# Performance work log

Measured on AMD Instinct MI355X. Metric: run time of the kernel, lower is better.

## Reference

```python
import jax, jax.numpy as jnp
import numpy as np

D, DFF, H, K = 512, 2048, 8, 31
DK = D // H
EPS = 1e-5


def _ln(x, g, b):
    m = jnp.mean(x, axis=-1, keepdims=True)
    v = jnp.mean((x - m) ** 2, axis=-1, keepdims=True)
    return (x - m) * jax.lax.rsqrt(v + EPS) * g + b


def _ffn(x, w1, b1, w2, b2):
    return jax.nn.silu(x @ w1 + b1) @ w2 + b2


def _rel_shift(x):
    # x: (B, H, T, P) with P = 2T-1
    b, h, q, p = x.shape
    x = jnp.pad(x, ((0, 0), (0, 0), (0, 0), (1, 0)))
    x = x.reshape(b, h, p + 1, q)[:, :, 1:, :]
    return x.reshape(b, h, q, p)


def setup_inputs() -> dict:
    key = jax.random.key(0)
    ks = jax.random.split(key, 32)
    r = lambda i, shape: 0.02 * jax.random.normal(ks[i], shape, dtype=jnp.float32)
    B, T = 4, 1024
    inp = {
        'x': jax.random.normal(ks[0], (B, T, D), dtype=jnp.float32),
        'pos_emb': jax.random.normal(ks[1], (1, 2 * T - 1, D), dtype=jnp.float32),
        # LayerNorms (5)
        'ln1_g': jnp.ones((D,)), 'ln1_b': jnp.zeros((D,)),
        'ln2_g': jnp.ones((D,)), 'ln2_b': jnp.zeros((D,)),
        'ln3_g': jnp.ones((D,)), 'ln3_b': jnp.zeros((D,)),
        'ln4_g': jnp.ones((D,)), 'ln4_b': jnp.zeros((D,)),
        'ln5_g': jnp.ones((D,)), 'ln5_b': jnp.zeros((D,)),
        # FFN1
        'ff1_w1': r(2, (D, DFF)), 'ff1_b1': jnp.zeros((DFF,)),
        'ff1_w2': r(3, (DFF, D)), 'ff1_b2': jnp.zeros((D,)),
        # Attention
        'wq': r(4, (D, D)), 'bq': jnp.zeros((D,)),
        'wk': r(5, (D, D)), 'bk': jnp.zeros((D,)),
        'wv': r(6, (D, D)), 'bv': jnp.zeros((D,)),
        'wp': r(7, (D, D)),
        'wo': r(8, (D, D)), 'bo': jnp.zeros((D,)),
        'pos_u': r(9, (H, DK)), 'pos_v': r(10, (H, DK)),
        # Conv module
        'pw1_w': r(11, (2 * D, D)), 'pw1_b': jnp.zeros((2 * D,)),
        'dw_w': r(12, (D, 1, K)), 'dw_b': jnp.zeros((D,)),
        'bn_g': jnp.ones((D,)), 'bn_b': jnp.zeros((D,)),
        'pw2_w': r(13, (D, D)), 'pw2_b': jnp.zeros((D,)),
        # FFN2
        'ff2_w1': r(14, (D, DFF)), 'ff2_b1': jnp.zeros((DFF,)),
        'ff2_w2': r(15, (DFF, D)), 'ff2_b2': jnp.zeros((D,)),
    }
    return inp


def _attn(x, pos_emb, wq, bq, wk, bk, wv, bv, wp, wo, bo, pos_u, pos_v):
    B, T, _ = x.shape
    q = (x @ wq + bq).reshape(B, T, H, DK).transpose(0, 2, 1, 3)
    k = (x @ wk + bk).reshape(B, T, H, DK).transpose(0, 2, 1, 3)
    v = (x @ wv + bv).reshape(B, T, H, DK).transpose(0, 2, 1, 3)
    P = pos_emb.shape[1]
    p = (pos_emb[0] @ wp).reshape(P, H, DK)  # (P, H, DK)
    ac = jnp.einsum('bhqd,bhkd->bhqk', q + pos_u[:, None, :], k)
    bd = jnp.einsum('bhqd,phd->bhqp', q + pos_v[:, None, :], p)
    bd = _rel_shift(bd)[:, :, :, :T]
    scores = (ac + bd) * (DK ** -0.5)
    attn = jax.nn.softmax(scores, axis=-1)
    out = jnp.einsum('bhqk,bhkd->bhqd', attn, v)
    out = out.transpose(0, 2, 1, 3).reshape(B, T, D)
    return out @ wo + bo


def _conv(x, pw1_w, pw1_b, dw_w, dw_b, bn_g, bn_b, pw2_w, pw2_b):
    y = x.transpose(0, 2, 1)  # (B, D, T)
    y = jnp.einsum('od,bdt->bot', pw1_w, y) + pw1_b[:, None]
    a, g = jnp.split(y, 2, axis=1)
    y = a * jax.nn.sigmoid(g)  # GLU
    pad = (K - 1) // 2
    y = jax.lax.conv_general_dilated(
        y, dw_w, (1,), [(pad, pad)],
        dimension_numbers=('NCW', 'OIW', 'NCW'), feature_group_count=D)
    y = y + dw_b[:, None]
    m = jnp.mean(y, axis=(0, 2), keepdims=True)
    var = jnp.mean((y - m) ** 2, axis=(0, 2), keepdims=True)
    y = (y - m) * jax.lax.rsqrt(var + EPS) * bn_g[:, None] + bn_b[:, None]
    y = jax.nn.silu(y)
    y = jnp.einsum('od,bdt->bot', pw2_w, y) + pw2_b[:, None]
    return y.transpose(0, 2, 1)


def reference(x, pos_emb,
              ln1_g, ln1_b, ff1_w1, ff1_b1, ff1_w2, ff1_b2,
              ln2_g, ln2_b, wq, bq, wk, bk, wv, bv, wp, wo, bo, pos_u, pos_v,
              ln3_g, ln3_b, pw1_w, pw1_b, dw_w, dw_b, bn_g, bn_b, pw2_w, pw2_b,
              ln4_g, ln4_b, ff2_w1, ff2_b1, ff2_w2, ff2_b2,
              ln5_g, ln5_b):
    h = x + 0.5 * _ffn(_ln(x, ln1_g, ln1_b), ff1_w1, ff1_b1, ff1_w2, ff1_b2)
    h = h + _attn(_ln(h, ln2_g, ln2_b), pos_emb, wq, bq, wk, bk, wv, bv, wp, wo, bo, pos_u, pos_v)
    h = h + _conv(_ln(h, ln3_g, ln3_b), pw1_w, pw1_b, dw_w, dw_b, bn_g, bn_b, pw2_w, pw2_b)
    h = h + 0.5 * _ffn(_ln(h, ln4_g, ln4_b), ff2_w1, ff2_b1, ff2_w2, ff2_b2)
    return _ln(h, ln5_g, ln5_b)
```

## Files before the change

### kernel.cpp

```cpp
#include <hip/hip_runtime.h>
#include <math.h>

#define TT   1024
#define BBZ  4
#define DD   512
#define DFF_ 2048
#define HH   8
#define DKK  64
#define NTOK 4096
#define EPSF 1e-5f
#define MB   1048576
#define QSCALE 0.18033688011112042f
#define M0OFF  24.0f

typedef unsigned short u16;
typedef __attribute__((ext_vector_type(8))) short s8v;
typedef __attribute__((ext_vector_type(4))) float f32x4;
typedef __attribute__((ext_vector_type(4))) unsigned short us4;

__device__ __forceinline__ float b2f(u16 v){
    union { unsigned int u; float f; } x; x.u = ((unsigned int)v) << 16; return x.f;
}
__device__ __forceinline__ u16 f2b(float f){
    union { float f; unsigned int u; } x; x.f = f;
    unsigned int r = x.u + 0x7fffu + ((x.u >> 16) & 1u);
    return (u16)(r >> 16);
}
__device__ __forceinline__ float sigmoidf_(float x){ return 1.0f/(1.0f+__expf(-x)); }

__device__ __forceinline__ void gld16(const u16* g, u16* l){
    __builtin_amdgcn_global_load_lds(
        (const __attribute__((address_space(1))) unsigned int*)g,
        (__attribute__((address_space(3))) unsigned int*)l, 16, 0, 0);
}

template<int OMODE>
__global__ __launch_bounds__(256) void bgemm128(
    const u16* __restrict__ A, int lda,
    const u16* __restrict__ B, int ldb,
    void* __restrict__ Cv, int ldc, int K,
    const float* __restrict__ bias, int act, float alpha,
    const float* __restrict__ resid,
    const float* __restrict__ posu, const float* __restrict__ posv)
{
    int n0 = blockIdx.x * 128;
    int m0 = blockIdx.y * 128;

    __shared__ u16 As[128*64];
    __shared__ u16 Bs[128*64];

    int t = threadIdx.x;
    int w = t >> 6, l = t & 63;
    int lrow = l >> 3, lslot = l & 7;
    int kswz = (lslot ^ lrow) * 8;
    int wm = w >> 1, wn = w & 1;
    int lr = l & 15, lk = l >> 4;

    f32x4 acc[4][4] = {};

    for (int k0 = 0; k0 < K; k0 += 64){
        #pragma unroll
        for (int it = 0; it < 4; ++it){
            int rb = it*32 + w*8;
            gld16(A + (size_t)(m0 + rb + lrow)*lda + k0 + kswz, &As[rb*64]);
            gld16(B + (size_t)(n0 + rb + lrow)*ldb + k0 + kswz, &Bs[rb*64]);
        }
        __syncthreads();

        s8v af[2][4], bf[2][4];
        #pragma unroll
        for (int kh = 0; kh < 2; ++kh){
            int sl = (kh*4 + lk) ^ (lr & 7);
            #pragma unroll
            for (int mi = 0; mi < 4; ++mi)
                af[kh][mi] = *(const s8v*)&As[(wm*64 + mi*16 + lr)*64 + sl*8];
            #pragma unroll
            for (int ni = 0; ni < 4; ++ni)
                bf[kh][ni] = *(const s8v*)&Bs[(wn*64 + ni*16 + lr)*64 + sl*8];
        }
        #pragma unroll
        for (int kh = 0; kh < 2; ++kh)
            #pragma unroll
            for (int mi = 0; mi < 4; ++mi)
                #pragma unroll
                for (int ni = 0; ni < 4; ++ni)
                    acc[mi][ni] = __builtin_amdgcn_mfma_f32_16x16x32_bf16(
                        af[kh][mi], bf[kh][ni], acc[mi][ni], 0, 0, 0);
        __syncthreads();
    }

    #pragma unroll
    for (int mi = 0; mi < 4; ++mi){
        #pragma unroll
        for (int ni = 0; ni < 4; ++ni){
            int gn = n0 + wn*64 + ni*16 + lr;
            float bval = bias ? bias[gn] : 0.0f;
            #pragma unroll
            for (int r = 0; r < 4; ++r){
                int gm = m0 + wm*64 + mi*16 + lk*4 + r;
                float vv = acc[mi][ni][r] + bval;
                if (act) vv = vv * sigmoidf_(vv);
                if (OMODE == 0){
                    vv *= alpha;
                    if (resid) vv += resid[(size_t)gm*ldc + gn];
                    ((float*)Cv)[(size_t)gm*ldc + gn] = vv;
                } else if (OMODE == 1){
                    ((u16*)Cv)[(size_t)gm*ldc + gn] = f2b(vv);
                } else if (OMODE == 5){
                    u16* base = (u16*)Cv;
                    if (gn < 512){
                        size_t idx = (size_t)gm*512 + gn;
                        base[idx]              = f2b((vv + posu[gn])*QSCALE);
                        base[idx + (2u<<20)]   = f2b((vv + posv[gn])*QSCALE);
                    } else if (gn < 1024){
                        base[(4u<<20) + (size_t)gm*512 + (gn-512)] = f2b(vv);
                    } else {
                        int gnp = gn - 1024;
                        int bb = gm >> 10, tt2 = gm & 1023;
                        size_t idx = (((size_t)(bb*8 + (gnp>>6)))*64 + (gnp&63))*1024 + tt2;
                        base[(6u<<20) + idx] = f2b(vv);
                    }
                } else {
                    u16* base = (u16*)Cv;
                    size_t idx = (gn < 512)
                        ? ((size_t)gm*512 + gn)*2
                        : ((size_t)gm*512 + (gn-512))*2 + 1;
                    base[idx] = f2b(vv);
                }
            }
        }
    }
}

template<int OMODE>
__global__ __launch_bounds__(256) void bgemm64(
    const u16* __restrict__ A, int lda,
    const u16* __restrict__ B, int ldb,
    void* __restrict__ Cv, int ldc, int K,
    const float* __restrict__ bias, float alpha,
    const float* __restrict__ resid)
{
    int n0 = blockIdx.x * 64;
    int m0 = blockIdx.y * 64;

    __shared__ u16 As[64*64];
    __shared__ u16 Bs[64*64];

    int t = threadIdx.x;
    int w = t >> 6, l = t & 63;
    int lrow = l >> 3, lslot = l & 7;
    int kswz = (lslot ^ lrow) * 8;
    int wm = w >> 1, wn = w & 1;
    int lr = l & 15, lk = l >> 4;

    f32x4 acc[2][2] = {};

    for (int k0 = 0; k0 < K; k0 += 64){
        #pragma unroll
        for (int it = 0; it < 2; ++it){
            int rb = it*32 + w*8;
            gld16(A + (size_t)(m0 + rb + lrow)*lda + k0 + kswz, &As[rb*64]);
            gld16(B + (size_t)(n0 + rb + lrow)*ldb + k0 + kswz, &Bs[rb*64]);
        }
        __syncthreads();

        s8v af[2][2], bf[2][2];
        #pragma unroll
        for (int kh = 0; kh < 2; ++kh){
            int sl = (kh*4 + lk) ^ (lr & 7);
            #pragma unroll
            for (int mi = 0; mi < 2; ++mi)
                af[kh][mi] = *(const s8v*)&As[(wm*32 + mi*16 + lr)*64 + sl*8];
            #pragma unroll
            for (int ni = 0; ni < 2; ++ni)
                bf[kh][ni] = *(const s8v*)&Bs[(wn*32 + ni*16 + lr)*64 + sl*8];
        }
        #pragma unroll
        for (int kh = 0; kh < 2; ++kh)
            #pragma unroll
            for (int mi = 0; mi < 2; ++mi)
                #pragma unroll
                for (int ni = 0; ni < 2; ++ni)
                    acc[mi][ni] = __builtin_amdgcn_mfma_f32_16x16x32_bf16(
                        af[kh][mi], bf[kh][ni], acc[mi][ni], 0, 0, 0);
        __syncthreads();
    }

    #pragma unroll
    for (int mi = 0; mi < 2; ++mi){
        #pragma unroll
        for (int ni = 0; ni < 2; ++ni){
            int gn = n0 + wn*32 + ni*16 + lr;
            float bval = bias ? bias[gn] : 0.0f;
            #pragma unroll
            for (int r = 0; r < 4; ++r){
                int gm = m0 + wm*32 + mi*16 + lk*4 + r;
                float vv = acc[mi][ni][r] + bval;
                if (OMODE == 0){
                    vv *= alpha;
                    if (resid) vv += resid[(size_t)gm*ldc + gn];
                    ((float*)Cv)[(size_t)gm*ldc + gn] = vv;
                } else {
                    ((u16*)Cv)[(size_t)gm*ldc + gn] = f2b(vv);
                }
            }
        }
    }
}

__global__ __launch_bounds__(256) void bgemm64k(
    const u16* __restrict__ A, int lda,
    const u16* __restrict__ B, int ldb,
    float* __restrict__ C, int ldc, int K,
    const float* __restrict__ bias, float alpha,
    const float* __restrict__ resid)
{
    int n0 = blockIdx.x * 64;
    int m0 = blockIdx.y * 64;

    __shared__ u16 As[64*128];
    __shared__ u16 Bs[64*128];

    int t = threadIdx.x;
    int w = t >> 6, l = t & 63;
    int r4 = l >> 4;
    int s16 = l & 15;
    int kswz = (s16 ^ (w*4 + r4)) * 8;
    int wm = w >> 1, wn = w & 1;
    int lr = l & 15, lk = l >> 4;

    f32x4 acc[2][2] = {};

    for (int k0 = 0; k0 < K; k0 += 128){
        #pragma unroll
        for (int cb = 0; cb < 4; ++cb){
            int rowu = cb*16 + w*4;
            gld16(A + (size_t)(m0 + rowu + r4)*lda + k0 + kswz, &As[rowu*128]);
            gld16(B + (size_t)(n0 + rowu + r4)*ldb + k0 + kswz, &Bs[rowu*128]);
        }
        __syncthreads();

        #pragma unroll
        for (int kh = 0; kh < 4; ++kh){
            int sl = ((kh*4 + lk) ^ lr) * 8;
            s8v af[2], bf[2];
            #pragma unroll
            for (int mi = 0; mi < 2; ++mi)
                af[mi] = *(const s8v*)&As[(wm*32 + mi*16 + lr)*128 + sl];
            #pragma unroll
            for (int ni = 0; ni < 2; ++ni)
                bf[ni] = *(const s8v*)&Bs[(wn*32 + ni*16 + lr)*128 + sl];
            #pragma unroll
            for (int mi = 0; mi < 2; ++mi)
                #pragma unroll
                for (int ni = 0; ni < 2; ++ni)
                    acc[mi][ni] = __builtin_amdgcn_mfma_f32_16x16x32_bf16(
                        af[mi], bf[ni], acc[mi][ni], 0, 0, 0);
        }
        __syncthreads();
    }

    #pragma unroll
    for (int mi = 0; mi < 2; ++mi){
        #pragma unroll
        for (int ni = 0; ni < 2; ++ni){
            int gn = n0 + wn*32 + ni*16 + lr;
            float bval = bias ? bias[gn] : 0.0f;
            #pragma unroll
            for (int r = 0; r < 4; ++r){
                int gm = m0 + wm*32 + mi*16 + lk*4 + r;
                float vv = (acc[mi][ni][r] + bval) * alpha;
                if (resid) vv += resid[(size_t)gm*ldc + gn];
                C[(size_t)gm*ldc + gn] = vv;
            }
        }
    }
}

__global__ __launch_bounds__(256) void attn_fused(
    const u16* __restrict__ qub, const u16* __restrict__ qvb,
    const u16* __restrict__ kb,  const u16* __restrict__ vt,
    const u16* __restrict__ pp,  u16* __restrict__ out)
{
    int z = blockIdx.y;
    int b = z >> 3, hh = z & 7;
    int i0 = blockIdx.x * 64;

    __shared__ u16 Kb2[2][64*64];
    __shared__ u16 Vb2[2][64*64];
    __shared__ u16 Pring[3][64*64];
    __shared__ u16 PT[64*64];
    __shared__ float Band[64*64];

    int t = threadIdx.x;
    int w = t >> 6, l = t & 63;
    int lrow = l >> 3, lslot = l & 7;
    int kswz = (lslot ^ lrow) * 8;
    int lr = l & 15, lk = l >> 4;

    #pragma unroll
    for (int it = 0; it < 2; ++it){
        int rb = it*32 + w*8;
        gld16(qub + (size_t)(b*TT + i0 + rb + lrow)*DD + hh*64 + kswz, &PT[rb*64]);
        gld16(qvb + (size_t)(b*TT + i0 + rb + lrow)*DD + hh*64 + kswz,
              (u16*)Band + rb*64);
    }
    __syncthreads();
    s8v af_u[2], af_v[2];
    #pragma unroll
    for (int kh = 0; kh < 2; ++kh){
        int sl = (kh*4 + lk) ^ (lr & 7);
        af_u[kh] = *(const s8v*)&PT[(w*16 + lr)*64 + sl*8];
        af_v[kh] = *(const s8v*)((const u16*)Band + (w*16 + lr)*64 + sl*8);
    }
    #pragma unroll
    for (int it = 0; it < 2; ++it){
        int rb = it*32 + w*8;
        gld16(kb + (size_t)(b*TT +        rb + lrow)*DD + hh*64 + kswz, &Kb2[0][rb*64]);
        gld16(vt + ((size_t)z*64 + rb + lrow)*TT +                kswz, &Vb2[0][rb*64]);
        gld16(pp + (size_t)(960  - i0 +   rb + lrow)*DD + hh*64 + kswz, &Pring[0][rb*64]);
        gld16(pp + (size_t)(1024 - i0 +   rb + lrow)*DD + hh*64 + kswz, &Pring[1][rb*64]);
    }

    f32x4 o_[4] = {};
    float Lp[4] = {0.f, 0.f, 0.f, 0.f};

    int nbase = 3 - w;
    int s0 = 0, s1 = 1, s2 = 2;

    for (int jt = 0; jt < 16; ++jt){
        int cur = jt & 1;
        __syncthreads();

        if (jt < 15){
            #pragma unroll
            for (int it = 0; it < 2; ++it){
                int rb = it*32 + w*8;
                gld16(kb + (size_t)(b*TT + (jt+1)*64 + rb + lrow)*DD + hh*64 + kswz,
                      &Kb2[cur^1][rb*64]);
                gld16(vt + ((size_t)z*64 + rb + lrow)*TT + (jt+1)*64 + kswz,
                      &Vb2[cur^1][rb*64]);
                gld16(pp + (size_t)(960 + (jt+2)*64 - i0 + rb + lrow)*DD + hh*64 + kswz,
                      &Pring[s2][rb*64]);
            }
        }

        f32x4 sac[4] = {};
        f32x4 g[5] = {};
        __builtin_amdgcn_s_setprio(1);
        #pragma unroll
        for (int kh = 0; kh < 2; ++kh){
            int sl = (kh*4 + lk) ^ (lr & 7);
            #pragma unroll
            for (int n = 0; n < 4; ++n){
                s8v bK = *(const s8v*)&Kb2[cur][(n*16 + lr)*64 + sl*8];
                sac[n] = __builtin_amdgcn_mfma_f32_16x16x32_bf16(af_u[kh], bK, sac[n], 0,0,0);
            }
            #pragma unroll
            for (int n = 0; n < 5; ++n){
                int nn = nbase + n;
                const u16* pc = (nn & 4) ? &Pring[s1][0] : &Pring[s0][0];
                s8v bP = *(const s8v*)&pc[(((nn&3)*16) + lr)*64 + sl*8];
                g[n] = __builtin_amdgcn_mfma_f32_16x16x32_bf16(af_v[kh], bP, g[n], 0,0,0);
            }
        }
        __builtin_amdgcn_s_setprio(0);
        #pragma unroll
        for (int n = 0; n < 5; ++n){
            int nn = nbase + n;
            #pragma unroll
            for (int r = 0; r < 4; ++r){
                int ii = w*16 + lk*4 + r;
                int jj = nn*16 + lr - 63 + ii;
                if (jj >= 0 && jj < 64)
                    Band[ii*64 + ((jj + 4*ii) & 63)] = g[n][r];
            }
        }

        float p_[4][4];
        #pragma unroll
        for (int r = 0; r < 4; ++r){
            int ii = w*16 + lk*4 + r;
            float rs = 0.0f;
            #pragma unroll
            for (int n = 0; n < 4; ++n){
                int jj = n*16 + lr;
                float s2 = sac[n][r] + Band[ii*64 + ((jj + 4*ii) & 63)];
                float pv = __builtin_amdgcn_exp2f(s2 - M0OFF);
                p_[n][r] = pv; rs += pv;
            }
            Lp[r] += rs;
        }

        #pragma unroll
        for (int n = 0; n < 4; ++n)
            #pragma unroll
            for (int r = 0; r < 4; ++r){
                int ii  = w*16 + lk*4 + r;
                int col = n*16 + lr;
                int sl  = (col>>3) ^ (ii&7);
                PT[ii*64 + sl*8 + (col&7)] = f2b(p_[n][r]);
            }

        __builtin_amdgcn_s_setprio(1);
        #pragma unroll
        for (int kh = 0; kh < 2; ++kh){
            int sl = (kh*4 + lk) ^ (lr & 7);
            s8v ap = *(const s8v*)&PT[(w*16 + lr)*64 + sl*8];
            #pragma unroll
            for (int n = 0; n < 4; ++n){
                s8v bV = *(const s8v*)&Vb2[cur][(n*16 + lr)*64 + sl*8];
                o_[n] = __builtin_amdgcn_mfma_f32_16x16x32_bf16(ap, bV, o_[n], 0,0,0);
            }
        }
        __builtin_amdgcn_s_setprio(0);
        int tmp = s0; s0 = s1; s1 = s2; s2 = tmp;
    }

    float Lr[4];
    #pragma unroll
    for (int r = 0; r < 4; ++r){
        float Lv = Lp[r];
        #pragma unroll
        for (int msk = 1; msk < 16; msk <<= 1) Lv += __shfl_xor(Lv, msk);
        Lr[r] = 1.0f / Lv;
    }

    #pragma unroll
    for (int n = 0; n < 4; ++n)
        #pragma unroll
        for (int r = 0; r < 4; ++r){
            int i  = i0 + w*16 + lk*4 + r;
            int dk = n*16 + lr;
            out[(size_t)(b*TT + i)*DD + hh*64 + dk] = f2b(o_[n][r] * Lr[r]);
        }
}

template<int OB>
__global__ __launch_bounds__(256) void ln_kernel(const float* __restrict__ in,
    const float* __restrict__ g, const float* __restrict__ b, void* __restrict__ outv)
{
    int w = threadIdx.x >> 6, l = threadIdx.x & 63;
    int row = blockIdx.x*4 + w;
    const float4* xr = (const float4*)(in + (size_t)row*DD);
    float4 v0 = xr[l], v1 = xr[64 + l];
    float s = v0.x+v0.y+v0.z+v0.w + v1.x+v1.y+v1.z+v1.w;
    float q = v0.x*v0.x+v0.y*v0.y+v0.z*v0.z+v0.w*v0.w
            + v1.x*v1.x+v1.y*v1.y+v1.z*v1.z+v1.w*v1.w;
    #pragma unroll
    for (int msk = 1; msk < 64; msk <<= 1){
        s += __shfl_xor(s, msk);
        q += __shfl_xor(q, msk);
    }
    float mean = s*(1.0f/DD);
    float var  = q*(1.0f/DD) - mean*mean;
    float inv  = rsqrtf(var+EPSF);
    float4 g0 = ((const float4*)g)[l], g1 = ((const float4*)g)[64+l];
    float4 b0 = ((const float4*)b)[l], b1 = ((const float4*)b)[64+l];
    float y0x=(v0.x-mean)*inv*g0.x+b0.x, y0y=(v0.y-mean)*inv*g0.y+b0.y;
    float y0z=(v0.z-mean)*inv*g0.z+b0.z, y0w=(v0.w-mean)*inv*g0.w+b0.w;
    float y1x=(v1.x-mean)*inv*g1.x+b1.x, y1y=(v1.y-mean)*inv*g1.y+b1.y;
    float y1z=(v1.z-mean)*inv*g1.z+b1.z, y1w=(v1.w-mean)*inv*g1.w+b1.w;
    if (OB){
        us4 o0 = { f2b(y0x), f2b(y0y), f2b(y0z), f2b(y0w) };
        us4 o1 = { f2b(y1x), f2b(y1y), f2b(y1z), f2b(y1w) };
        us4* op = (us4*)((u16*)outv + (size_t)row*DD);
        op[l] = o0; op[64+l] = o1;
    } else {
        float4 o0 = { y0x, y0y, y0z, y0w };
        float4 o1 = { y1x, y1y, y1z, y1w };
        float4* op = (float4*)((float*)outv + (size_t)row*DD);
        op[l] = o0; op[64+l] = o1;
    }
}

struct Prep9 {
    const float* s[9];
    u16* d[9];
    int R[9], C[9];
    int t0[10];
};

__global__ __launch_bounds__(256) void prep_transpose(Prep9 P)
{
    __shared__ float tile[32][33];
    int bid = blockIdx.x;
    int j = 0;
    #pragma unroll
    for (int e=1; e<9; e++) if (bid >= P.t0[e]) j = e;
    int lb = bid - P.t0[j];
    int nx = P.C[j] >> 5;
    int c0 = (lb % nx) << 5;
    int r0 = (lb / nx) << 5;
    const float* in = P.s[j];
    u16* out = P.d[j];
    int R = P.R[j], C = P.C[j];
    int tx = threadIdx.x & 31, ty = threadIdx.x >> 5;
    #pragma unroll
    for (int i=0;i<4;i++){
        int rr = ty + i*8;
        tile[rr][tx] = in[(size_t)(r0+rr)*C + c0+tx];
    }
    __syncthreads();
    #pragma unroll
    for (int i=0;i<4;i++){
        int cc = ty + i*8;
        out[(size_t)(c0+cc)*R + r0+tx] = f2b(tile[tx][cc]);
    }
}

__global__ __launch_bounds__(256) void prep_convert(
    const float* __restrict__ pw1_w, const float* __restrict__ pw2_w,
    const float* __restrict__ pos_emb, const float* __restrict__ dw_w,
    const float* __restrict__ bq, const float* __restrict__ bk,
    const float* __restrict__ bv,
    u16* __restrict__ pw1b, u16* __restrict__ pw2b,
    u16* __restrict__ posb, float* __restrict__ wt, float* __restrict__ bqkv)
{
    int i = blockIdx.x*256 + threadIdx.x;
    if (i < 524288) { pw1b[i] = f2b(pw1_w[i]); return; }
    i -= 524288;
    if (i < 262144) { pw2b[i] = f2b(pw2_w[i]); return; }
    i -= 262144;
    if (i < 1048576) { posb[i] = (i < 2047*512) ? f2b(pos_emb[i]) : (u16)0; return; }
    i -= 1048576;
    if (i < 15872) { int kk = i >> 9, d = i & 511; wt[i] = dw_w[d*31+kk]; return; }
    i -= 15872;
    if (i < 1536) bqkv[i] = (i < 512) ? bq[i] : (i < 1024 ? bk[i-512] : bv[i-1024]);
}

__global__ __launch_bounds__(256) void dwconv_kernel(const unsigned int* __restrict__ t2i,
    const float* __restrict__ wt, const float* __restrict__ bias, u16* __restrict__ z)
{
    int d  = blockIdx.x*256 + threadIdx.x;
    int c  = blockIdx.y;
    int b  = c >> 7;
    int t0 = (c & 127) << 3;
    const unsigned int* pa = t2i + (size_t)b*TT*512 + d;
    float wv[31];
    #pragma unroll
    for (int kk=0;kk<31;kk++) wv[kk] = wt[kk*512 + d];
    float xv[38];
    #pragma unroll
    for (int e=0;e<38;e++){
        int tp = t0 - 15 + e;
        if (tp >= 0 && tp < TT){
            unsigned int pv = pa[(size_t)tp*512];
            float a  = b2f((u16)(pv & 0xffffu));
            float gg = b2f((u16)(pv >> 16));
            xv[e] = a * sigmoidf_(gg);
        } else xv[e] = 0.0f;
    }
    float bsv = bias[d];
    #pragma unroll
    for (int j=0;j<8;j++){
        float sum = bsv;
        #pragma unroll
        for (int kk=0;kk<31;kk++) sum = fmaf(xv[j+kk], wv[kk], sum);
        z[(size_t)(b*TT+t0+j)*DD + d] = f2b(sum);
    }
}

__global__ __launch_bounds__(256) void bn_reduce2(const u16* __restrict__ z,
    float* __restrict__ stats)
{
    int bi = blockIdx.x;
    int t  = threadIdx.x;
    float s0=0.f,q0=0.f,s1=0.f,q1=0.f;
    #pragma unroll
    for (int r=0;r<16;r++){
        size_t row = (size_t)(bi*16 + r)*DD;
        float v0 = b2f(z[row + t]);
        float v1 = b2f(z[row + t + 256]);
        s0 += v0; q0 += v0*v0;
        s1 += v1; q1 += v1*v1;
    }
    atomicAdd(&stats[t],        s0);
    atomicAdd(&stats[512 + t],  q0);
    atomicAdd(&stats[t + 256],      s1);
    atomicAdd(&stats[512 + t + 256], q1);
}

__global__ __launch_bounds__(256) void bn_apply_kernel(const u16* __restrict__ z,
    const float* __restrict__ stats, const float* __restrict__ g, const float* __restrict__ b,
    u16* __restrict__ out)
{
    int idx = blockIdx.x*256 + threadIdx.x;
    int c = idx & (DD-1);
    float m   = stats[c]*(1.0f/NTOK);
    float var = stats[DD+c]*(1.0f/NTOK) - m*m;
    float vv  = (b2f(z[idx])-m)*rsqrtf(var+EPSF)*g[c] + b[c];
    out[idx]  = f2b(vv*sigmoidf_(vv));
}

extern "C" void kernel_launch(void* const* d_in, const int* in_sizes, int n_in,
                              void* d_out, int out_size, void* d_ws, size_t ws_size,
                              hipStream_t stream)
{
    const float* x       = (const float*)d_in[0];
    const float* pos_emb = (const float*)d_in[1];
    const float* ln1_g=(const float*)d_in[2],  *ln1_b=(const float*)d_in[3];
    const float* ln2_g=(const float*)d_in[4],  *ln2_b=(const float*)d_in[5];
    const float* ln3_g=(const float*)d_in[6],  *ln3_b=(const float*)d_in[7];
    const float* ln4_g=(const float*)d_in[8],  *ln4_b=(const float*)d_in[9];
    const float* ln5_g=(const float*)d_in[10], *ln5_b=(const float*)d_in[11];
    const float* ff1_w1=(const float*)d_in[12], *ff1_b1=(const float*)d_in[13];
    const float* ff1_w2=(const float*)d_in[14], *ff1_b2=(const float*)d_in[15];
    const float* wq=(const float*)d_in[16], *bq=(const float*)d_in[17];
    const float* wk=(const float*)d_in[18], *bk=(const float*)d_in[19];
    const float* wv=(const float*)d_in[20], *bv=(const float*)d_in[21];
    const float* wp=(const float*)d_in[22];
    const float* wo=(const float*)d_in[23], *bo=(const float*)d_in[24];
    const float* pos_u=(const float*)d_in[25], *pos_v=(const float*)d_in[26];
    const float* pw1_w=(const float*)d_in[27], *pw1_b=(const float*)d_in[28];
    const float* dw_w=(const float*)d_in[29],  *dw_b=(const float*)d_in[30];
    const float* bn_g=(const float*)d_in[31],  *bn_b=(const float*)d_in[32];
    const float* pw2_w=(const float*)d_in[33], *pw2_b=(const float*)d_in[34];
    const float* ff2_w1=(const float*)d_in[35], *ff2_b1=(const float*)d_in[36];
    const float* ff2_w2=(const float*)d_in[37], *ff2_b2=(const float*)d_in[38];

    char* W = (char*)d_ws;
    float* h    = (float*)(W);
    u16*  xn    = (u16*) (W + (size_t) 8*MB);
    u16*  wall  = (u16*) (W + (size_t)12*MB);
    u16*  qub   = (u16*) (W + (size_t)28*MB);
    u16*  qvb   = (u16*) (W + (size_t)32*MB);
    u16*  kb    = (u16*) (W + (size_t)36*MB);
    u16*  vt    = (u16*) (W + (size_t)40*MB);
    u16*  pproj = (u16*) (W + (size_t)44*MB);
    char* big   = W + (size_t)48*MB;
    u16*  ffh   = (u16*)big;
    unsigned int* t2i = (unsigned int*)big;
    u16*  t3u   = (u16*)(big + (size_t)8*MB);
    float* stats= (float*)(W + (size_t)112*MB);
    float* wt   = stats + 4096;
    float* bqkv = wt + 15872;

    u16* ff1w1T = wall;
    u16* ff1w2T = wall + 1048576;
    u16* wqT    = wall + 2097152;
    u16* wkT    = wall + 2359296;
    u16* wvT    = wall + 2621440;
    u16* wpT    = wall + 2883584;
    u16* woT    = wall + 3145728;
    u16* ff2w1T = wall + 3407872;
    u16* ff2w2T = wall + 4456448;
    u16* pw1b   = wall + 5505024;
    u16* pw2b   = wall + 6029312;
    u16* posb   = wall + 6291456;

    dim3 blk(256);

    Prep9 P;
    P.s[0]=ff1_w1; P.d[0]=ff1w1T; P.R[0]=512;  P.C[0]=2048;
    P.s[1]=ff1_w2; P.d[1]=ff1w2T; P.R[1]=2048; P.C[1]=512;
    P.s[2]=wq;     P.d[2]=wqT;    P.R[2]=512;  P.C[2]=512;
    P.s[3]=wk;     P.d[3]=wkT;    P.R[3]=512;  P.C[3]=512;
    P.s[4]=wv;     P.d[4]=wvT;    P.R[4]=512;  P.C[4]=512;
    P.s[5]=wp;     P.d[5]=wpT;    P.R[5]=512;  P.C[5]=512;
    P.s[6]=wo;     P.d[6]=woT;    P.R[6]=512;  P.C[6]=512;
    P.s[7]=ff2_w1; P.d[7]=ff2w1T; P.R[7]=512;  P.C[7]=2048;
    P.s[8]=ff2_w2; P.d[8]=ff2w2T; P.R[8]=2048; P.C[8]=512;
    int tc[9] = {1024,1024,256,256,256,256,256,1024,1024};
    P.t0[0]=0; for (int e=0;e<9;e++) P.t0[e+1]=P.t0[e]+tc[e];
    prep_transpose<<<dim3(5376), blk, 0, stream>>>(P);
    prep_convert<<<dim3(7236), blk, 0, stream>>>(pw1_w, pw2_w, pos_emb, dw_w,
                                                 bq, bk, bv,
                                                 pw1b, pw2b, posb, wt, bqkv);

    ln_kernel<1><<<dim3(NTOK/4), blk, 0, stream>>>(x, ln1_g, ln1_b, xn);
    bgemm128<1><<<dim3(16,32), blk, 0, stream>>>(xn,512, ff1w1T,512,
        ffh,2048, 512, ff1_b1,1,1.f, nullptr,nullptr,nullptr);
    bgemm64k<<<dim3(8,64), blk, 0, stream>>>(ffh,2048, ff1w2T,2048,
        h,512, 2048, ff1_b2,0.5f, x);

    ln_kernel<1><<<dim3(NTOK/4), blk, 0, stream>>>(h, ln2_g, ln2_b, xn);
    bgemm128<5><<<dim3(12,32), blk, 0, stream>>>(xn,512, wqT,512,
        qub,512, 512, bqkv,0,1.f, nullptr,pos_u,pos_v);
    bgemm64<1><<<dim3(8,32), blk, 0, stream>>>(posb,512, wpT,512,
        pproj,512, 512, nullptr,1.f, nullptr);

    attn_fused<<<dim3(16,32), blk, 0, stream>>>(qub, qvb, kb, vt, pproj, xn);

    bgemm64<0><<<dim3(8,64), blk, 0, stream>>>(xn,512, woT,512,
        h,512, 512, bo,1.f, h);

    ln_kernel<1><<<dim3(NTOK/4), blk, 0, stream>>>(h, ln3_g, ln3_b, xn);
    bgemm128<6><<<dim3(8,32), blk, 0, stream>>>(xn,512, pw1b,512,
        t2i,1024, 512, pw1_b,0,1.f, nullptr,nullptr,nullptr);
    dwconv_kernel<<<dim3(2,512), blk, 0, stream>>>(t2i, wt, dw_b, t3u);
    hipMemsetAsync(stats, 0, 4096, stream);
    bn_reduce2<<<dim3(256), blk, 0, stream>>>(t3u, stats);
    bn_apply_kernel<<<dim3(NTOK*DD/256), blk, 0, stream>>>(t3u, stats, bn_g, bn_b, xn);
    bgemm64<0><<<dim3(8,64), blk, 0, stream>>>(xn,512, pw2b,512,
        h,512, 512, pw2_b,1.f, h);

    ln_kernel<1><<<dim3(NTOK/4), blk, 0, stream>>>(h, ln4_g, ln4_b, xn);
    bgemm128<1><<<dim3(16,32), blk, 0, stream>>>(xn,512, ff2w1T,512,
        ffh,2048, 512, ff2_b1,1,1.f, nullptr,nullptr,nullptr);
    bgemm64k<<<dim3(8,64), blk, 0, stream>>>(ffh,2048, ff2w2T,2048,
        h,512, 2048, ff2_b2,0.5f, h);

    ln_kernel<0><<<dim3(NTOK/4), blk, 0, stream>>>(h, ln5_g, ln5_b, (float*)d_out);
}
```

Measured before the change: 279.1 us.

## Store residual stream in bf16, merge prep kernels, rework attention band layout

The residual stream h is now kept in bf16 rather than fp32. The GEMM epilogues read and write bf16 residuals, and the layernorm kernel gains a bf16-input variant with 8-wide vector loads. The two weight-prep kernels are merged into one launch. The attention kernel's positional band scratch is reorganised into per-warp diagonal-indexed buffers with vectorised f32x4 stores, replacing scattered scalar stores. Keeping the residual in bf16 roughly halves its memory traffic, but repeated rounding adds accuracy risk.

New measurement: 276.7 us. Within noise of the previous version (-0.9%).

```diff
diff --git a/kernel.cpp b/kernel.cpp
--- a/kernel.cpp
+++ b/kernel.cpp
@@ -17,6 +17,7 @@
 typedef __attribute__((ext_vector_type(8))) short s8v;
 typedef __attribute__((ext_vector_type(4))) float f32x4;
 typedef __attribute__((ext_vector_type(4))) unsigned short us4;
+typedef __attribute__((ext_vector_type(8))) unsigned short us8;
 
 __device__ __forceinline__ float b2f(u16 v){
     union { unsigned int u; float f; } x; x.u = ((unsigned int)v) << 16; return x.f;
@@ -39,8 +40,7 @@
     const u16* __restrict__ A, int lda,
     const u16* __restrict__ B, int ldb,
     void* __restrict__ Cv, int ldc, int K,
-    const float* __restrict__ bias, int act, float alpha,
-    const float* __restrict__ resid,
+    const float* __restrict__ bias, int act,
     const float* __restrict__ posu, const float* __restrict__ posv)
 {
     int n0 = blockIdx.x * 128;
@@ -100,11 +100,7 @@
                 int gm = m0 + wm*64 + mi*16 + lk*4 + r;
                 float vv = acc[mi][ni][r] + bval;
                 if (act) vv = vv * sigmoidf_(vv);
-                if (OMODE == 0){
-                    vv *= alpha;
-                    if (resid) vv += resid[(size_t)gm*ldc + gn];
-                    ((float*)Cv)[(size_t)gm*ldc + gn] = vv;
-                } else if (OMODE == 1){
+                if (OMODE == 1){
                     ((u16*)Cv)[(size_t)gm*ldc + gn] = f2b(vv);
                 } else if (OMODE == 5){
                     u16* base = (u16*)Cv;
@@ -136,9 +132,9 @@
 __global__ __launch_bounds__(256) void bgemm64(
     const u16* __restrict__ A, int lda,
     const u16* __restrict__ B, int ldb,
-    void* __restrict__ Cv, int ldc, int K,
+    u16* __restrict__ C, int ldc, int K,
     const float* __restrict__ bias, float alpha,
-    const float* __restrict__ resid)
+    const u16* __restrict__ resid)
 {
     int n0 = blockIdx.x * 64;
     int m0 = blockIdx.y * 64;
@@ -198,11 +194,9 @@
                 float vv = acc[mi][ni][r] + bval;
                 if (OMODE == 0){
                     vv *= alpha;
-                    if (resid) vv += resid[(size_t)gm*ldc + gn];
-                    ((float*)Cv)[(size_t)gm*ldc + gn] = vv;
-                } else {
-                    ((u16*)Cv)[(size_t)gm*ldc + gn] = f2b(vv);
+                    if (resid) vv += b2f(resid[(size_t)gm*ldc + gn]);
                 }
+                C[(size_t)gm*ldc + gn] = f2b(vv);
             }
         }
     }
@@ -211,9 +205,9 @@
 __global__ __launch_bounds__(256) void bgemm64k(
     const u16* __restrict__ A, int lda,
     const u16* __restrict__ B, int ldb,
-    float* __restrict__ C, int ldc, int K,
+    u16* __restrict__ C, int ldc, int K,
     const float* __restrict__ bias, float alpha,
-    const float* __restrict__ resid)
+    const float* __restrict__ residF, const u16* __restrict__ residB)
 {
     int n0 = blockIdx.x * 64;
     int m0 = blockIdx.y * 64;
@@ -270,8 +264,10 @@
             for (int r = 0; r < 4; ++r){
                 int gm = m0 + wm*32 + mi*16 + lk*4 + r;
                 float vv = (acc[mi][ni][r] + bval) * alpha;
-                if (resid) vv += resid[(size_t)gm*ldc + gn];
-                C[(size_t)gm*ldc + gn] = vv;
+                size_t idx = (size_t)gm*ldc + gn;
+                if (residF) vv += residF[idx];
+                if (residB) vv += b2f(residB[idx]);
+                C[idx] = f2b(vv);
             }
         }
     }
@@ -290,7 +286,7 @@
     __shared__ u16 Vb2[2][64*64];
     __shared__ u16 Pring[3][64*64];
     __shared__ u16 PT[64*64];
-    __shared__ float Band[64*64];
+    __shared__ float Bandd[4][1024];
 
     int t = threadIdx.x;
     int w = t >> 6, l = t & 63;
@@ -303,7 +299,7 @@
         int rb = it*32 + w*8;
         gld16(qub + (size_t)(b*TT + i0 + rb + lrow)*DD + hh*64 + kswz, &PT[rb*64]);
         gld16(qvb + (size_t)(b*TT + i0 + rb + lrow)*DD + hh*64 + kswz,
-              (u16*)Band + rb*64);
+              (u16*)&Bandd[0][0] + rb*64);
     }
     __syncthreads();
     s8v af_u[2], af_v[2];
@@ -311,7 +307,7 @@
     for (int kh = 0; kh < 2; ++kh){
         int sl = (kh*4 + lk) ^ (lr & 7);
         af_u[kh] = *(const s8v*)&PT[(w*16 + lr)*64 + sl*8];
-        af_v[kh] = *(const s8v*)((const u16*)Band + (w*16 + lr)*64 + sl*8);
+        af_v[kh] = *(const s8v*)((const u16*)&Bandd[0][0] + (w*16 + lr)*64 + sl*8);
     }
     #pragma unroll
     for (int it = 0; it < 2; ++it){
@@ -325,7 +321,6 @@
     f32x4 o_[4] = {};
     float Lp[4] = {0.f, 0.f, 0.f, 0.f};
 
-    int nbase = 3 - w;
     int s0 = 0, s1 = 1, s2 = 2;
 
     for (int jt = 0; jt < 16; ++jt){
@@ -358,35 +353,45 @@
             }
             #pragma unroll
             for (int n = 0; n < 5; ++n){
-                int nn = nbase + n;
+                int nn = (3 - w) + n;
                 const u16* pc = (nn & 4) ? &Pring[s1][0] : &Pring[s0][0];
                 s8v bP = *(const s8v*)&pc[(((nn&3)*16) + lr)*64 + sl*8];
                 g[n] = __builtin_amdgcn_mfma_f32_16x16x32_bf16(af_v[kh], bP, g[n], 0,0,0);
             }
         }
         __builtin_amdgcn_s_setprio(0);
-        #pragma unroll
-        for (int n = 0; n < 5; ++n){
-            int nn = nbase + n;
+
+        {
+            int c0 = (3 - w)*16 + lr;
+            int d  = (c0 - 63) & 63;
+            int sb = (lk*4 + ((d >> 1) & 3)*4) & 15;
+            f32x4 vv;
             #pragma unroll
             for (int r = 0; r < 4; ++r){
-                int ii = w*16 + lk*4 + r;
-                int jj = nn*16 + lr - 63 + ii;
-                if (jj >= 0 && jj < 64)
-                    Band[ii*64 + ((jj + 4*ii) & 63)] = g[n][r];
-            }
+                int iia = w*16 + lk*4 + r;
+                vv[r] = (iia >= 63 - c0) ? g[0][r] : g[4][r];
+            }
+            *(f32x4*)&Bandd[w][d*16 + sb] = vv;
+        }
+        #pragma unroll
+        for (int n = 1; n < 4; ++n){
+            int c = (3 - w + n)*16 + lr;
+            int d = (c - 63) & 63;
+            int sb = (lk*4 + ((d >> 1) & 3)*4) & 15;
+            *(f32x4*)&Bandd[w][d*16 + sb] = g[n];
         }
 
         float p_[4][4];
         #pragma unroll
         for (int r = 0; r < 4; ++r){
-            int ii = w*16 + lk*4 + r;
+            int ii_l = lk*4 + r;
             float rs = 0.0f;
             #pragma unroll
             for (int n = 0; n < 4; ++n){
                 int jj = n*16 + lr;
-                float s2 = sac[n][r] + Band[ii*64 + ((jj + 4*ii) & 63)];
-                float pv = __builtin_amdgcn_exp2f(s2 - M0OFF);
+                int d  = (jj - 16*w - ii_l) & 63;
+                float bd = Bandd[w][d*16 + ((ii_l + ((d>>1)&3)*4) & 15)];
+                float pv = __builtin_amdgcn_exp2f(sac[n][r] + bd - M0OFF);
                 p_[n][r] = pv; rs += pv;
             }
             Lp[r] += rs;
@@ -436,17 +441,26 @@
         }
 }
 
-template<int OB>
-__global__ __launch_bounds__(256) void ln_kernel(const float* __restrict__ in,
+template<int IB, int OB>
+__global__ __launch_bounds__(256) void ln_kernel(const void* __restrict__ inp,
     const float* __restrict__ g, const float* __restrict__ b, void* __restrict__ outv)
 {
     int w = threadIdx.x >> 6, l = threadIdx.x & 63;
     int row = blockIdx.x*4 + w;
-    const float4* xr = (const float4*)(in + (size_t)row*DD);
-    float4 v0 = xr[l], v1 = xr[64 + l];
-    float s = v0.x+v0.y+v0.z+v0.w + v1.x+v1.y+v1.z+v1.w;
-    float q = v0.x*v0.x+v0.y*v0.y+v0.z*v0.z+v0.w*v0.w
-            + v1.x*v1.x+v1.y*v1.y+v1.z*v1.z+v1.w*v1.w;
+    float v[8];
+    if (IB){
+        us8 xv = ((const us8*)((const u16*)inp + (size_t)row*DD))[l];
+        #pragma unroll
+        for (int e=0;e<8;e++) v[e] = b2f(xv[e]);
+    } else {
+        const float4* xr = (const float4*)((const float*)inp + (size_t)row*DD);
+        float4 a = xr[2*l], c = xr[2*l+1];
+        v[0]=a.x; v[1]=a.y; v[2]=a.z; v[3]=a.w;
+        v[4]=c.x; v[5]=c.y; v[6]=c.z; v[7]=c.w;
+    }
+    float s = 0.f, q = 0.f;
+    #pragma unroll
+    for (int e=0;e<8;e++){ s += v[e]; q += v[e]*v[e]; }
     #pragma unroll
     for (int msk = 1; msk < 64; msk <<= 1){
         s += __shfl_xor(s, msk);
@@ -454,23 +468,24 @@
     }
     float mean = s*(1.0f/DD);
     float var  = q*(1.0f/DD) - mean*mean;
-    float inv  = rsqrtf(var+EPSF);
-    float4 g0 = ((const float4*)g)[l], g1 = ((const float4*)g)[64+l];
-    float4 b0 = ((const float4*)b)[l], b1 = ((const float4*)b)[64+l];
-    float y0x=(v0.x-mean)*inv*g0.x+b0.x, y0y=(v0.y-mean)*inv*g0.y+b0.y;
-    float y0z=(v0.z-mean)*inv*g0.z+b0.z, y0w=(v0.w-mean)*inv*g0.w+b0.w;
-    float y1x=(v1.x-mean)*inv*g1.x+b1.x, y1y=(v1.y-mean)*inv*g1.y+b1.y;
-    float y1z=(v1.z-mean)*inv*g1.z+b1.z, y1w=(v1.w-mean)*inv*g1.w+b1.w;
+    float rinv = rsqrtf(var+EPSF);
+    float4 g0 = ((const float4*)g)[2*l], g1 = ((const float4*)g)[2*l+1];
+    float4 b0 = ((const float4*)b)[2*l], b1 = ((const float4*)b)[2*l+1];
+    float gv[8] = {g0.x,g0.y,g0.z,g0.w,g1.x,g1.y,g1.z,g1.w};
+    float bv[8] = {b0.x,b0.y,b0.z,b0.w,b1.x,b1.y,b1.z,b1.w};
+    float y[8];
+    #pragma unroll
+    for (int e=0;e<8;e++) y[e] = (v[e]-mean)*rinv*gv[e] + bv[e];
     if (OB){
-        us4 o0 = { f2b(y0x), f2b(y0y), f2b(y0z), f2b(y0w) };
-        us4 o1 = { f2b(y1x), f2b(y1y), f2b(y1z), f2b(y1w) };
-        us4* op = (us4*)((u16*)outv + (size_t)row*DD);
-        op[l] = o0; op[64+l] = o1;
+        us8 o;
+        #pragma unroll
+        for (int e=0;e<8;e++) o[e] = f2b(y[e]);
+        ((us8*)((u16*)outv + (size_t)row*DD))[l] = o;
     } else {
-        float4 o0 = { y0x, y0y, y0z, y0w };
-        float4 o1 = { y1x, y1y, y1z, y1w };
+        float4 o0 = {y[0],y[1],y[2],y[3]};
+        float4 o1 = {y[4],y[5],y[6],y[7]};
         float4* op = (float4*)((float*)outv + (size_t)row*DD);
-        op[l] = o0; op[64+l] = o1;
+        op[2*l] = o0; op[2*l+1] = o1;
     }
 }
 
@@ -481,35 +496,7 @@
     int t0[10];
 };
 
-__global__ __launch_bounds__(256) void prep_transpose(Prep9 P)
-{
-    __shared__ float tile[32][33];
-    int bid = blockIdx.x;
-    int j = 0;
-    #pragma unroll
-    for (int e=1; e<9; e++) if (bid >= P.t0[e]) j = e;
-    int lb = bid - P.t0[j];
-    int nx = P.C[j] >> 5;
-    int c0 = (lb % nx) << 5;
-    int r0 = (lb / nx) << 5;
-    const float* in = P.s[j];
-    u16* out = P.d[j];
-    int R = P.R[j], C = P.C[j];
-    int tx = threadIdx.x & 31, ty = threadIdx.x >> 5;
-    #pragma unroll
-    for (int i=0;i<4;i++){
-        int rr = ty + i*8;
-        tile[rr][tx] = in[(size_t)(r0+rr)*C + c0+tx];
-    }
-    __syncthreads();
-    #pragma unroll
-    for (int i=0;i<4;i++){
-        int cc = ty + i*8;
-        out[(size_t)(c0+cc)*R + r0+tx] = f2b(tile[tx][cc]);
-    }
-}
-
-__global__ __launch_bounds__(256) void prep_convert(
+__global__ __launch_bounds__(256) void prep_all(Prep9 P,
     const float* __restrict__ pw1_w, const float* __restrict__ pw2_w,
     const float* __restrict__ pos_emb, const float* __restrict__ dw_w,
     const float* __restrict__ bq, const float* __restrict__ bk,
@@ -517,7 +504,34 @@
     u16* __restrict__ pw1b, u16* __restrict__ pw2b,
     u16* __restrict__ posb, float* __restrict__ wt, float* __restrict__ bqkv)
 {
-    int i = blockIdx.x*256 + threadIdx.x;
+    __shared__ float tile[32][33];
+    int bid = blockIdx.x;
+    if (bid < 5376){
+        int j = 0;
+        #pragma unroll
+        for (int e=1; e<9; e++) if (bid >= P.t0[e]) j = e;
+        int lb = bid - P.t0[j];
+        int nx = P.C[j] >> 5;
+        int c0 = (lb % nx) << 5;
+        int r0 = (lb / nx) << 5;
+        const float* in = P.s[j];
+        u16* out = P.d[j];
+        int R = P.R[j], C = P.C[j];
+        int tx = threadIdx.x & 31, ty = threadIdx.x >> 5;
+        #pragma unroll
+        for (int i=0;i<4;i++){
+            int rr = ty + i*8;
+            tile[rr][tx] = in[(size_t)(r0+rr)*C + c0+tx];
+        }
+        __syncthreads();
+        #pragma unroll
+        for (int i=0;i<4;i++){
+            int cc = ty + i*8;
+            out[(size_t)(c0+cc)*R + r0+tx] = f2b(tile[tx][cc]);
+        }
+        return;
+    }
+    int i = (bid - 5376)*256 + threadIdx.x;
     if (i < 524288) { pw1b[i] = f2b(pw1_w[i]); return; }
     i -= 524288;
     if (i < 262144) { pw2b[i] = f2b(pw2_w[i]); return; }
@@ -620,7 +634,7 @@
     const float* ff2_w2=(const float*)d_in[37], *ff2_b2=(const float*)d_in[38];
 
     char* W = (char*)d_ws;
-    float* h    = (float*)(W);
+    u16*  h     = (u16*) (W);
     u16*  xn    = (u16*) (W + (size_t) 8*MB);
     u16*  wall  = (u16*) (W + (size_t)12*MB);
     u16*  qub   = (u16*) (W + (size_t)28*MB);
@@ -663,20 +677,19 @@
     P.s[8]=ff2_w2; P.d[8]=ff2w2T; P.R[8]=2048; P.C[8]=512;
     int tc[9] = {1024,1024,256,256,256,256,256,1024,1024};
     P.t0[0]=0; for (int e=0;e<9;e++) P.t0[e+1]=P.t0[e]+tc[e];
-    prep_transpose<<<dim3(5376), blk, 0, stream>>>(P);
-    prep_convert<<<dim3(7236), blk, 0, stream>>>(pw1_w, pw2_w, pos_emb, dw_w,
-                                                 bq, bk, bv,
-                                                 pw1b, pw2b, posb, wt, bqkv);
-
-    ln_kernel<1><<<dim3(NTOK/4), blk, 0, stream>>>(x, ln1_g, ln1_b, xn);
+    prep_all<<<dim3(5376+7236), blk, 0, stream>>>(P, pw1_w, pw2_w, pos_emb, dw_w,
+                                                  bq, bk, bv,
+                                                  pw1b, pw2b, posb, wt, bqkv);
+
+    ln_kernel<0,1><<<dim3(NTOK/4), blk, 0, stream>>>(x, ln1_g, ln1_b, xn);
     bgemm128<1><<<dim3(16,32), blk, 0, stream>>>(xn,512, ff1w1T,512,
-        ffh,2048, 512, ff1_b1,1,1.f, nullptr,nullptr,nullptr);
+        ffh,2048, 512, ff1_b1,1, nullptr,nullptr);
     bgemm64k<<<dim3(8,64), blk, 0, stream>>>(ffh,2048, ff1w2T,2048,
-        h,512, 2048, ff1_b2,0.5f, x);
-
-    ln_kernel<1><<<dim3(NTOK/4), blk, 0, stream>>>(h, ln2_g, ln2_b, xn);
+        h,512, 2048, ff1_b2,0.5f, x, nullptr);
+
+    ln_kernel<1,1><<<dim3(NTOK/4), blk, 0, stream>>>(h, ln2_g, ln2_b, xn);
     bgemm128<5><<<dim3(12,32), blk, 0, stream>>>(xn,512, wqT,512,
-        qub,512, 512, bqkv,0,1.f, nullptr,pos_u,pos_v);
+        qub,512, 512, bqkv,0, pos_u,pos_v);
     bgemm64<1><<<dim3(8,32), blk, 0, stream>>>(posb,512, wpT,512,
         pproj,512, 512, nullptr,1.f, nullptr);
 
@@ -685,21 +698,21 @@
     bgemm64<0><<<dim3(8,64), blk, 0, stream>>>(xn,512, woT,512,
         h,512, 512, bo,1.f, h);
 
-    ln_kernel<1><<<dim3(NTOK/4), blk, 0, stream>>>(h, ln3_g, ln3_b, xn);
+    ln_kernel<1,1><<<dim3(NTOK/4), blk, 0, stream>>>(h, ln3_g, ln3_b, xn);
     bgemm128<6><<<dim3(8,32), blk, 0, stream>>>(xn,512, pw1b,512,
-        t2i,1024, 512, pw1_b,0,1.f, nullptr,nullptr,nullptr);
+        t2i,1024, 512, pw1_b,0, nullptr,nullptr);
     dwconv_kernel<<<dim3(2,512), blk, 0, stream>>>(t2i, wt, dw_b, t3u);
-    hipMemsetAsync(stats, 0, 4096, stream);
+    (void)hipMemsetAsync(stats, 0, 4096, stream);
     bn_reduce2<<<dim3(256), blk, 0, stream>>>(t3u, stats);
     bn_apply_kernel<<<dim3(NTOK*DD/256), blk, 0, stream>>>(t3u, stats, bn_g, bn_b, xn);
     bgemm64<0><<<dim3(8,64), blk, 0, stream>>>(xn,512, pw2b,512,
         h,512, 512, pw2_b,1.f, h);
 
-    ln_kernel<1><<<dim3(NTOK/4), blk, 0, stream>>>(h, ln4_g, ln4_b, xn);
+    ln_kernel<1,1><<<dim3(NTOK/4), blk, 0, stream>>>(h, ln4_g, ln4_b, xn);
     bgemm128<1><<<dim3(16,32), blk, 0, stream>>>(xn,512, ff2w1T,512,
-        ffh,2048, 512, ff2_b1,1,1.f, nullptr,nullptr,nullptr);
+        ffh,2048, 512, ff2_b1,1, nullptr,nullptr);
     bgemm64k<<<dim3(8,64), blk, 0, stream>>>(ffh,2048, ff2w2T,2048,
-        h,512, 2048, ff2_b2,0.5f, h);
-
-    ln_kernel<0><<<dim3(NTOK/4), blk, 0, stream>>>(h, ln5_g, ln5_b, (float*)d_out);
-}
+        h,512, 2048, ff2_b2,0.5f, nullptr, h);
+
+    ln_kernel<1,0><<<dim3(NTOK/4), blk, 0, stream>>>(h, ln5_g, ln5_b, (float*)d_out);
+}
```
